# Kernel tuning notes

Hardware: AMD Instinct MI355X
Metric: run time of the kernel (lower is better)

Reference implementation:

```python
import jax, jax.numpy as jnp
import numpy as np

EPS = 1e-12

def _agnn(x, src, dst, beta, n):
    # L2-normalize node features (F.normalize semantics: clamp norm at eps)
    norm = jnp.maximum(jnp.linalg.norm(x, axis=-1, keepdims=True), EPS)
    xn = x / norm
    # cosine similarity per edge, scaled by learnable beta
    a = beta * jnp.sum(xn[dst] * xn[src], axis=-1)  # [E]
    # numerically-stable softmax over incoming edges of each target node
    amax = jax.ops.segment_max(a, dst, num_segments=n)            # [N]
    e = jnp.exp(a - amax[dst])                                     # [E]
    denom = jax.ops.segment_sum(e, dst, num_segments=n)           # [N]
    alpha = e / jnp.maximum(denom[dst], EPS)                       # [E]
    # weighted scatter-add aggregation of source features
    return jax.ops.segment_sum(alpha[:, None] * x[src], dst, num_segments=n)


def setup_inputs() -> dict:
    key = jax.random.key(0)
    ks = jax.random.split(key, 6)
    N, E, F_in, C = 50000, 800000, 1024, 256
    x = jax.random.normal(ks[0], (N, F_in), dtype=jnp.float32)
    edge_index = jax.random.randint(ks[1], (2, E), 0, N, dtype=jnp.int64)
    lin1_w = jax.random.normal(ks[2], (64, F_in), dtype=jnp.float32) / np.sqrt(F_in)
    lin1_b = jax.random.normal(ks[3], (64,), dtype=jnp.float32) * 0.01
    beta1 = jnp.ones((1,), dtype=jnp.float32)
    beta2 = jnp.ones((1,), dtype=jnp.float32)
    lin2_w = jax.random.normal(ks[4], (C, 64), dtype=jnp.float32) / np.sqrt(64.0)
    lin2_b = jax.random.normal(ks[5], (C,), dtype=jnp.float32) * 0.01
    return {"x": x, "edge_index": edge_index, "lin1_w": lin1_w, "lin1_b": lin1_b,
            "beta1": beta1, "beta2": beta2, "lin2_w": lin2_w, "lin2_b": lin2_b}


def reference(x, edge_index, lin1_w, lin1_b, beta1, beta2, lin2_w, lin2_b):
    n = x.shape[0]
    src, dst = edge_index[0], edge_index[1]  # PyG: row0 = source j, row1 = target i
    # dropout is identity in eval mode
    h = jax.nn.relu(jnp.einsum('nf,hf->nh', x, lin1_w) + lin1_b)  # [N, 64]
    h = _agnn(h, src, dst, beta1[0], n)
    h = _agnn(h, src, dst, beta2[0], n)
    logits = jnp.einsum('nh,ch->nc', h, lin2_w) + lin2_b          # [N, C]
    return jax.nn.log_softmax(logits, axis=1)
```

## Files before the change

kernel.cpp:

```cpp
#include <hip/hip_runtime.h>
#include <hip/hip_bf16.h>

#define EPSF 1e-12f
#define CAP 64

typedef __attribute__((ext_vector_type(8))) short short8;
typedef __attribute__((ext_vector_type(4))) float f32x4;

__device__ __forceinline__ short f2bf(float f) {
    union { float f; unsigned u; } v; v.f = f;
    unsigned r = v.u + 0x7fffu + ((v.u >> 16) & 1u);
    return (short)(r >> 16);
}
__device__ __forceinline__ float bf2f(ushort u) {
    return __uint_as_float((unsigned)u << 16);
}
__device__ __forceinline__ void gload_lds16(const void* g, void* l) {
    __builtin_amdgcn_global_load_lds(
        (const __attribute__((address_space(1))) void*)g,
        (__attribute__((address_space(3))) void*)l, 16, 0, 0);
}

__global__ __launch_bounds__(256) void prep_kernel(const float4* __restrict__ W1,
                                                   const float4* __restrict__ W2,
                                                   ushort* __restrict__ W1b,
                                                   ushort* __restrict__ W2b,
                                                   int* __restrict__ cnt, int N) {
    int i = blockIdx.x * 256 + threadIdx.x;
    const float4* Wp; ushort* Wo; int idx;
    if (i < 16384) { Wp = W1; Wo = W1b; idx = i; }
    else           { Wp = W2; Wo = W2b; idx = i - 16384; }
    float4 v = Wp[idx];
    ushort4 o;
    o.x = (ushort)f2bf(v.x); o.y = (ushort)f2bf(v.y);
    o.z = (ushort)f2bf(v.z); o.w = (ushort)f2bf(v.w);
    *(ushort4*)(Wo + 4 * (size_t)idx) = o;
    int n4 = N >> 2;
    if (i < n4) ((int4*)cnt)[i] = make_int4(0, 0, 0, 0);
}

__global__ __launch_bounds__(256) void lin1_scatter_kernel(const float* __restrict__ x,
                                                           const ushort* __restrict__ Wb,
                                                           const float* __restrict__ b,
                                                           ushort* __restrict__ xnb,
                                                           float* __restrict__ nrm_out,
                                                           const int* __restrict__ src,
                                                           const int* __restrict__ dst,
                                                           int* __restrict__ cnt,
                                                           ushort* __restrict__ esrcb,
                                                           int nLin1, int N, int E) {
    __shared__ char slds[4][2][4096];
    const int bid = (int)blockIdx.x;

    if (bid >= nLin1) {
        int e = (bid - nLin1) * 256 + threadIdx.x;
        if (e < E) {
            int d = dst[e];
            int p = atomicAdd(&cnt[d], 1);
            if (p < CAP) esrcb[(d << 6) + p] = (ushort)src[e];
        }
        return;
    }

    const int lane = threadIdx.x & 63;
    const int wv = threadIdx.x >> 6;
    const int rbase = bid * 64 + wv * 16;
    const int r15 = lane & 15;
    const int kg = lane >> 4;
    const int rsw = (r15 & 7) << 5;

    const char* xb = (const char*)x;
    const int irow4 = lane >> 4;
    const int icl = lane & 15;
    const ushort* wbase = Wb + (size_t)r15 * 1024 + kg * 8;

#define ISSUE_CHUNK(c, buf)                                                         \
    {                                                                               \
        _Pragma("unroll")                                                           \
        for (int j = 0; j < 4; ++j) {                                               \
            int rl = 4 * j + irow4;                                                 \
            int rg = rbase + rl; if (rg >= N) rg = N - 1;                           \
            gload_lds16(xb + (size_t)rg * 4096 + (c) * 256 +                        \
                            ((icl * 16) ^ ((rl & 7) << 5)),                         \
                        &slds[wv][buf][j * 1024]);                                  \
        }                                                                           \
    }

    f32x4 acc[4];
#pragma unroll
    for (int t = 0; t < 4; ++t) acc[t] = (f32x4){0.f, 0.f, 0.f, 0.f};

    short8 Wreg[2][8];

    ISSUE_CHUNK(0, 0)
    ISSUE_CHUNK(1, 1)
#pragma unroll
    for (int t = 0; t < 4; ++t)
#pragma unroll
        for (int kl = 0; kl < 2; ++kl)
            Wreg[0][t * 2 + kl] = *(const short8*)(wbase + (size_t)t * 16384 + kl * 32);

#pragma unroll
    for (int c = 0; c < 16; ++c) {
        if (c < 15) { asm volatile("s_waitcnt vmcnt(4)" ::: "memory"); }
        else        { asm volatile("s_waitcnt vmcnt(0)" ::: "memory"); }
        __builtin_amdgcn_sched_barrier(0);

        if (c + 1 < 16) {
#pragma unroll
            for (int t = 0; t < 4; ++t)
#pragma unroll
                for (int kl = 0; kl < 2; ++kl)
                    Wreg[(c + 1) & 1][t * 2 + kl] =
                        *(const short8*)(wbase + (size_t)t * 16384 +
                                         ((c + 1) * 2 + kl) * 32);
        }

        const char* arow = &slds[wv][c & 1][0] + r15 * 256;
#pragma unroll
        for (int kl = 0; kl < 2; ++kl) {
            int lc = (kg * 32 + kl * 128) ^ rsw;
            float4 f0 = *(const float4*)(arow + lc);
            float4 f1 = *(const float4*)(arow + lc + 16);
            short8 af;
            af[0] = f2bf(f0.x); af[1] = f2bf(f0.y); af[2] = f2bf(f0.z); af[3] = f2bf(f0.w);
            af[4] = f2bf(f1.x); af[5] = f2bf(f1.y); af[6] = f2bf(f1.z); af[7] = f2bf(f1.w);
#pragma unroll
            for (int t = 0; t < 4; ++t)
                acc[t] = __builtin_amdgcn_mfma_f32_16x16x32_bf16(af, Wreg[c & 1][t * 2 + kl],
                                                                 acc[t], 0, 0, 0);
        }
        asm volatile("s_waitcnt lgkmcnt(0)" ::: "memory");
        __builtin_amdgcn_sched_barrier(0);
        if (c + 2 < 16) ISSUE_CHUNK(c + 2, c & 1)
    }
#undef ISSUE_CHUNK

    float bb[4];
#pragma unroll
    for (int t = 0; t < 4; ++t) bb[t] = b[t * 16 + r15];

#pragma unroll
    for (int reg = 0; reg < 4; ++reg) {
        float hv[4];
        float ss = 0.f;
#pragma unroll
        for (int t = 0; t < 4; ++t) {
            hv[t] = fmaxf(acc[t][reg] + bb[t], 0.f);
            ss += hv[t] * hv[t];
        }
        ss += __shfl_xor(ss, 1); ss += __shfl_xor(ss, 2);
        ss += __shfl_xor(ss, 4); ss += __shfl_xor(ss, 8);
        float nrm = fmaxf(sqrtf(ss), EPSF);
        int node = rbase + kg * 4 + reg;
        if (node < N) {
            float ri = 1.f / nrm;
#pragma unroll
            for (int t = 0; t < 4; ++t)
                xnb[(size_t)node * 64 + t * 16 + r15] = (ushort)f2bf(hv[t] * ri);
            if (r15 == 0) nrm_out[node] = nrm;
        }
    }
}

__global__ __launch_bounds__(256) void agnn_fused_kernel(const ushort* __restrict__ xnb,
                                                         const float* __restrict__ nrm,
                                                         const int* __restrict__ cnt,
                                                         const ushort* __restrict__ esrcb,
                                                         const float* __restrict__ beta,
                                                         ushort* __restrict__ xnb_out,
                                                         float* __restrict__ nrm_out, int N) {
    const int lane = threadIdx.x & 63;
    const int l = lane & 15;
    int node = (blockIdx.x * 256 + threadIdx.x) >> 4;
    bool valid = node < N;
    int nodec = valid ? node : N - 1;

    int deg = cnt[nodec]; if (deg > CAP) deg = CAP;
    const ushort* eb = esrcb + (nodec << 6);
    ushort4 xd4 = *(const ushort4*)(xnb + (size_t)nodec * 64 + 4 * l);
    float xd0 = bf2f(xd4.x), xd1 = bf2f(xd4.y), xd2 = bf2f(xd4.z), xd3 = bf2f(xd4.w);
    float bet = beta[0];

    float sum = 0.f;
    float4 acc = make_float4(0.f, 0.f, 0.f, 0.f);

    int k = 0;
    int nf = (deg >= 4) ? 1 : 0;
    int p0 = 0, p1 = 0, p2 = 0, p3 = 0;
    if (nf) { p0 = eb[0]; p1 = eb[1]; p2 = eb[2]; p3 = eb[3]; }
    for (; k + 3 < deg; k += 4) {
        int s0i = p0, s1i = p1, s2i = p2, s3i = p3;
        if (k + 7 < deg) { p0 = eb[k+4]; p1 = eb[k+5]; p2 = eb[k+6]; p3 = eb[k+7]; }
        ushort4 v0 = *(const ushort4*)(xnb + (size_t)s0i * 64 + 4 * l);
        ushort4 v1 = *(const ushort4*)(xnb + (size_t)s1i * 64 + 4 * l);
        ushort4 v2 = *(const ushort4*)(xnb + (size_t)s2i * 64 + 4 * l);
        ushort4 v3 = *(const ushort4*)(xnb + (size_t)s3i * 64 + 4 * l);
        float n0 = nrm[s0i], n1 = nrm[s1i], n2 = nrm[s2i], n3 = nrm[s3i];
        float a0 = bf2f(v0.x), a1 = bf2f(v0.y), a2 = bf2f(v0.z), a3 = bf2f(v0.w);
        float b0 = bf2f(v1.x), b1 = bf2f(v1.y), b2 = bf2f(v1.z), b3 = bf2f(v1.w);
        float c0 = bf2f(v2.x), c1 = bf2f(v2.y), c2 = bf2f(v2.z), c3 = bf2f(v2.w);
        float d0 = bf2f(v3.x), d1 = bf2f(v3.y), d2 = bf2f(v3.z), d3 = bf2f(v3.w);
        float pa = a0 * xd0 + a1 * xd1 + a2 * xd2 + a3 * xd3;
        float pb = b0 * xd0 + b1 * xd1 + b2 * xd2 + b3 * xd3;
        float pc = c0 * xd0 + c1 * xd1 + c2 * xd2 + c3 * xd3;
        float pd = d0 * xd0 + d1 * xd1 + d2 * xd2 + d3 * xd3;
        pa += __shfl_xor(pa, 1); pb += __shfl_xor(pb, 1);
        pc += __shfl_xor(pc, 1); pd += __shfl_xor(pd, 1);
        pa += __shfl_xor(pa, 2); pb += __shfl_xor(pb, 2);
        pc += __shfl_xor(pc, 2); pd += __shfl_xor(pd, 2);
        pa += __shfl_xor(pa, 4); pb += __shfl_xor(pb, 4);
        pc += __shfl_xor(pc, 4); pd += __shfl_xor(pd, 4);
        pa += __shfl_xor(pa, 8); pb += __shfl_xor(pb, 8);
        pc += __shfl_xor(pc, 8); pd += __shfl_xor(pd, 8);
        float wa = __expf(bet * pa), wb = __expf(bet * pb);
        float wc = __expf(bet * pc), wd = __expf(bet * pd);
        float wna = wa * n0, wnb = wb * n1, wnc = wc * n2, wnd = wd * n3;
        sum += (wa + wb) + (wc + wd);
        acc.x += wna * a0 + wnb * b0 + wnc * c0 + wnd * d0;
        acc.y += wna * a1 + wnb * b1 + wnc * c1 + wnd * d1;
        acc.z += wna * a2 + wnb * b2 + wnc * c2 + wnd * d2;
        acc.w += wna * a3 + wnb * b3 + wnc * c3 + wnd * d3;
    }
    for (; k < deg; ++k) {
        int sa = eb[k];
        ushort4 va = *(const ushort4*)(xnb + (size_t)sa * 64 + 4 * l);
        float na = nrm[sa];
        float a0 = bf2f(va.x), a1 = bf2f(va.y), a2 = bf2f(va.z), a3 = bf2f(va.w);
        float pa = a0 * xd0 + a1 * xd1 + a2 * xd2 + a3 * xd3;
        pa += __shfl_xor(pa, 1); pa += __shfl_xor(pa, 2);
        pa += __shfl_xor(pa, 4); pa += __shfl_xor(pa, 8);
        float wa = __expf(bet * pa);
        float wna = wa * na;
        sum += wa;
        acc.x += wna * a0; acc.y += wna * a1;
        acc.z += wna * a2; acc.w += wna * a3;
    }

    float r = 1.f / fmaxf(sum, EPSF);
    float ox = acc.x * r, oy = acc.y * r, oz = acc.z * r, ow = acc.w * r;
    if (valid) {
        if (nrm_out) {
            float ss = ox * ox + oy * oy + oz * oz + ow * ow;
            ss += __shfl_xor(ss, 1); ss += __shfl_xor(ss, 2);
            ss += __shfl_xor(ss, 4); ss += __shfl_xor(ss, 8);
            float nr = fmaxf(sqrtf(ss), EPSF);
            float ri = 1.f / nr;
            ushort4 ob;
            ob.x = (ushort)f2bf(ox * ri); ob.y = (ushort)f2bf(oy * ri);
            ob.z = (ushort)f2bf(oz * ri); ob.w = (ushort)f2bf(ow * ri);
            *(ushort4*)(xnb_out + (size_t)node * 64 + 4 * l) = ob;
            if (l == 0) nrm_out[node] = nr;
        } else {
            ushort4 ob;
            ob.x = (ushort)f2bf(ox); ob.y = (ushort)f2bf(oy);
            ob.z = (ushort)f2bf(oz); ob.w = (ushort)f2bf(ow);
            *(ushort4*)(xnb_out + (size_t)node * 64 + 4 * l) = ob;
        }
    }
}

__global__ __launch_bounds__(256) void lin2_mfma_ls_kernel(const ushort* __restrict__ h2b,
                                                           const ushort* __restrict__ W2b,
                                                           const float* __restrict__ b,
                                                           float* __restrict__ out, int N) {
    const int lane = threadIdx.x & 63;
    const int wv = threadIdx.x >> 6;
    const int nbase = blockIdx.x * 64 + wv * 16;
    const int r15 = lane & 15;
    const int kg = lane >> 4;

    int an = nbase + r15; if (an >= N) an = N - 1;
    const ushort* ap = h2b + (size_t)an * 64 + kg * 8;
    short8 a0 = *(const short8*)(ap);
    short8 a1 = *(const short8*)(ap + 32);

    f32x4 acc[16];
#pragma unroll
    for (int t = 0; t < 16; ++t) {
        const ushort* wp = W2b + (size_t)(t * 16 + r15) * 64 + kg * 8;
        short8 b0 = *(const short8*)(wp);
        short8 b1 = *(const short8*)(wp + 32);
        acc[t] = __builtin_amdgcn_mfma_f32_16x16x32_bf16(a0, b0, (f32x4){0.f,0.f,0.f,0.f}, 0, 0, 0);
        acc[t] = __builtin_amdgcn_mfma_f32_16x16x32_bf16(a1, b1, acc[t], 0, 0, 0);
    }

#pragma unroll
    for (int t = 0; t < 16; ++t) {
        float bc = b[t * 16 + r15];
        acc[t][0] += bc; acc[t][1] += bc; acc[t][2] += bc; acc[t][3] += bc;
    }

#pragma unroll
    for (int r = 0; r < 4; ++r) {
        float mx = -1e30f;
#pragma unroll
        for (int t = 0; t < 16; ++t) mx = fmaxf(mx, acc[t][r]);
        mx = fmaxf(mx, __shfl_xor(mx, 1)); mx = fmaxf(mx, __shfl_xor(mx, 2));
        mx = fmaxf(mx, __shfl_xor(mx, 4)); mx = fmaxf(mx, __shfl_xor(mx, 8));
        float s = 0.f;
#pragma unroll
        for (int t = 0; t < 16; ++t) s += __expf(acc[t][r] - mx);
        s += __shfl_xor(s, 1); s += __shfl_xor(s, 2);
        s += __shfl_xor(s, 4); s += __shfl_xor(s, 8);
        float lse = mx + __logf(s);
        int node = nbase + kg * 4 + r;
        if (node < N) {
            float* op = out + (size_t)node * 256 + r15;
#pragma unroll
            for (int t = 0; t < 16; ++t) op[t * 16] = acc[t][r] - lse;
        }
    }
}

extern "C" void kernel_launch(void* const* d_in, const int* in_sizes, int n_in,
                              void* d_out, int out_size, void* d_ws, size_t ws_size,
                              hipStream_t stream) {
    const float* x      = (const float*)d_in[0];
    const int*   ei     = (const int*)d_in[1];
    const float* W1     = (const float*)d_in[2];
    const float* b1     = (const float*)d_in[3];
    const float* beta1  = (const float*)d_in[4];
    const float* beta2  = (const float*)d_in[5];
    const float* W2     = (const float*)d_in[6];
    const float* b2     = (const float*)d_in[7];
    float* out = (float*)d_out;

    const int N = in_sizes[0] / 1024;
    const int E = in_sizes[1] / 2;
    const int* src = ei;
    const int* dst = ei + E;

    char* ws = (char*)d_ws;
    const size_t XB = (size_t)N * 64 * sizeof(ushort);
    ushort* xn0b = (ushort*)(ws);
    ushort* xn1b = (ushort*)(ws + XB);
    ushort* h2b  = (ushort*)(ws + 2 * XB);
    size_t off = 3 * XB;
    float* norm0  = (float*)(ws + off); off += (size_t)N * sizeof(float);
    float* norm1  = (float*)(ws + off); off += (size_t)N * sizeof(float);
    int*   cnt    = (int*)(ws + off);   off += (size_t)N * sizeof(int);
    off = (off + 255) & ~(size_t)255;
    ushort* esrcb = (ushort*)(ws + off); off += (size_t)N * CAP * sizeof(ushort);
    ushort* W1b   = (ushort*)(ws + off); off += 64 * 1024 * sizeof(ushort);
    ushort* W2b   = (ushort*)(ws + off); off += 256 * 64 * sizeof(ushort);

    const int gLin1 = (N + 63) / 64;
    const int gE    = (E + 255) / 256;
    const int gNode = (N + 15) / 16;
    const int gLin2 = (N + 63) / 64;

    prep_kernel<<<80, 256, 0, stream>>>((const float4*)W1, (const float4*)W2,
                                        W1b, W2b, cnt, N);
    lin1_scatter_kernel<<<gLin1 + gE, 256, 0, stream>>>(x, W1b, b1, xn0b, norm0,
                                                        src, dst, cnt, esrcb,
                                                        gLin1, N, E);

    agnn_fused_kernel<<<gNode, 256, 0, stream>>>(xn0b, norm0, cnt, esrcb, beta1,
                                                 xn1b, norm1, N);
    agnn_fused_kernel<<<gNode, 256, 0, stream>>>(xn1b, norm1, cnt, esrcb, beta2,
                                                 h2b, nullptr, N);

    lin2_mfma_ls_kernel<<<gLin2, 256, 0, stream>>>(h2b, W2b, b2, out, N);
}
```

Measured before the change: 183.0 us.

## Load lin1 A-operand directly from global into registers instead of LDS staging

Replaces the global_load_lds double-buffered staging of x tiles through shared memory with direct per-lane float4 loads into registers, software-pipelined one k-step ahead alongside the W loads. This removes LDS traffic, the swizzle and the explicit waitcnt/sched barriers. In exchange, each lane reads 32-byte fragments strided across rows, so global coalescing is worse. Prefetch depth also drops from two chunks to one k-step, which may expose more memory latency on this bandwidth-bound GEMM.

```diff
diff --git a/kernel.cpp b/kernel.cpp
--- a/kernel.cpp
+++ b/kernel.cpp
@@ -14,11 +14,6 @@
 }
 __device__ __forceinline__ float bf2f(ushort u) {
     return __uint_as_float((unsigned)u << 16);
-}
-__device__ __forceinline__ void gload_lds16(const void* g, void* l) {
-    __builtin_amdgcn_global_load_lds(
-        (const __attribute__((address_space(1))) void*)g,
-        (__attribute__((address_space(3))) void*)l, 16, 0, 0);
 }
 
 __global__ __launch_bounds__(256) void prep_kernel(const float4* __restrict__ W1,
@@ -49,7 +44,6 @@
                                                            int* __restrict__ cnt,
                                                            ushort* __restrict__ esrcb,
                                                            int nLin1, int N, int E) {
-    __shared__ char slds[4][2][4096];
     const int bid = (int)blockIdx.x;
 
     if (bid >= nLin1) {
@@ -67,74 +61,45 @@
     const int rbase = bid * 64 + wv * 16;
     const int r15 = lane & 15;
     const int kg = lane >> 4;
-    const int rsw = (r15 & 7) << 5;
-
-    const char* xb = (const char*)x;
-    const int irow4 = lane >> 4;
-    const int icl = lane & 15;
+
+    int arow = rbase + r15; if (arow >= N) arow = N - 1;
+    const float* xp = x + (size_t)arow * 1024 + kg * 8;
     const ushort* wbase = Wb + (size_t)r15 * 1024 + kg * 8;
 
-#define ISSUE_CHUNK(c, buf)                                                         \
-    {                                                                               \
-        _Pragma("unroll")                                                           \
-        for (int j = 0; j < 4; ++j) {                                               \
-            int rl = 4 * j + irow4;                                                 \
-            int rg = rbase + rl; if (rg >= N) rg = N - 1;                           \
-            gload_lds16(xb + (size_t)rg * 4096 + (c) * 256 +                        \
-                            ((icl * 16) ^ ((rl & 7) << 5)),                         \
-                        &slds[wv][buf][j * 1024]);                                  \
-        }                                                                           \
-    }
-
     f32x4 acc[4];
 #pragma unroll
     for (int t = 0; t < 4; ++t) acc[t] = (f32x4){0.f, 0.f, 0.f, 0.f};
 
-    short8 Wreg[2][8];
-
-    ISSUE_CHUNK(0, 0)
-    ISSUE_CHUNK(1, 1)
+    float4 xa[2][2];
+    short8 Wreg[2][4];
+
+    xa[0][0] = *(const float4*)(xp);
+    xa[0][1] = *(const float4*)(xp + 4);
 #pragma unroll
     for (int t = 0; t < 4; ++t)
-#pragma unroll
-        for (int kl = 0; kl < 2; ++kl)
-            Wreg[0][t * 2 + kl] = *(const short8*)(wbase + (size_t)t * 16384 + kl * 32);
-
-#pragma unroll
-    for (int c = 0; c < 16; ++c) {
-        if (c < 15) { asm volatile("s_waitcnt vmcnt(4)" ::: "memory"); }
-        else        { asm volatile("s_waitcnt vmcnt(0)" ::: "memory"); }
-        __builtin_amdgcn_sched_barrier(0);
-
-        if (c + 1 < 16) {
+        Wreg[0][t] = *(const short8*)(wbase + (size_t)t * 16384);
+
+#pragma unroll
+    for (int k0 = 0; k0 < 32; ++k0) {
+        const int cur = k0 & 1, nxt = cur ^ 1;
+        if (k0 + 1 < 32) {
+            xa[nxt][0] = *(const float4*)(xp + (k0 + 1) * 32);
+            xa[nxt][1] = *(const float4*)(xp + (k0 + 1) * 32 + 4);
 #pragma unroll
             for (int t = 0; t < 4; ++t)
-#pragma unroll
-                for (int kl = 0; kl < 2; ++kl)
-                    Wreg[(c + 1) & 1][t * 2 + kl] =
-                        *(const short8*)(wbase + (size_t)t * 16384 +
-                                         ((c + 1) * 2 + kl) * 32);
-        }
-
-        const char* arow = &slds[wv][c & 1][0] + r15 * 256;
-#pragma unroll
-        for (int kl = 0; kl < 2; ++kl) {
-            int lc = (kg * 32 + kl * 128) ^ rsw;
-            float4 f0 = *(const float4*)(arow + lc);
-            float4 f1 = *(const float4*)(arow + lc + 16);
-            short8 af;
-            af[0] = f2bf(f0.x); af[1] = f2bf(f0.y); af[2] = f2bf(f0.z); af[3] = f2bf(f0.w);
-            af[4] = f2bf(f1.x); af[5] = f2bf(f1.y); af[6] = f2bf(f1.z); af[7] = f2bf(f1.w);
-#pragma unroll
-            for (int t = 0; t < 4; ++t)
-                acc[t] = __builtin_amdgcn_mfma_f32_16x16x32_bf16(af, Wreg[c & 1][t * 2 + kl],
-                                                                 acc[t], 0, 0, 0);
-        }
-        asm volatile("s_waitcnt lgkmcnt(0)" ::: "memory");
-        __builtin_amdgcn_sched_barrier(0);
-        if (c + 2 < 16) ISSUE_CHUNK(c + 2, c & 1)
-    }
-#undef ISSUE_CHUNK
+                Wreg[nxt][t] = *(const short8*)(wbase + (size_t)t * 16384 +
+                                                (k0 + 1) * 32);
+        }
+        short8 af;
+        af[0] = f2bf(xa[cur][0].x); af[1] = f2bf(xa[cur][0].y);
+        af[2] = f2bf(xa[cur][0].z); af[3] = f2bf(xa[cur][0].w);
+        af[4] = f2bf(xa[cur][1].x); af[5] = f2bf(xa[cur][1].y);
+        af[6] = f2bf(xa[cur][1].z); af[7] = f2bf(xa[cur][1].w);
+#pragma unroll
+        for (int t = 0; t < 4; ++t)
+            acc[t] = __builtin_amdgcn_mfma_f32_16x16x32_bf16(af, Wreg[cur][t],
+                                                             acc[t], 0, 0, 0);
+    }
 
     float bb[4];
 #pragma unroll
```

New measurement: 210.0 us. 14.8% more time.
